# Kernel tuning notes

Hardware: AMD Instinct MI355X
Metric: run time of the kernel (lower is better)

The kernel has to match this reference:

```python
import jax, jax.numpy as jnp
import numpy as np

B, T, C = 2, 2048, 768
H, N_LEFT = 12, 6
D = C // H


def setup_inputs() -> dict:
    key = jax.random.key(0)
    ks = jax.random.split(key, 4)
    x = jax.random.normal(ks[0], (B, T, C), dtype=jnp.float32)
    attention_mask = jnp.ones((B, T), dtype=jnp.int32)
    Wqkv_w = jax.random.normal(ks[1], (3 * C, C), dtype=jnp.float32) * (C ** -0.5)
    Wqkv_b = jnp.zeros((3 * C,), dtype=jnp.float32)
    Wo_w = jax.random.normal(ks[2], (C, C), dtype=jnp.float32) * (C ** -0.5)
    Wo_b = jnp.zeros((C,), dtype=jnp.float32)
    return {"x": x, "attention_mask": attention_mask, "Wqkv_w": Wqkv_w,
            "Wqkv_b": Wqkv_b, "Wo_w": Wo_w, "Wo_b": Wo_b}


def _attend(q, k, v, mask):
    # q,k,v: [B,h,T,D]; mask: [B,1,T,T] additive
    s = jnp.einsum('bhqd,bhkd->bhqk', q, k) * (D ** -0.5) + mask
    a = jax.nn.softmax(s.astype(jnp.float32), axis=-1).astype(q.dtype)
    return jnp.einsum('bhqk,bhkd->bhqd', a, v)


def reference(x, attention_mask, Wqkv_w, Wqkv_b, Wo_w, Wo_b):
    neg = jnp.finfo(x.dtype).min
    # padding mask [B,1,1,T]: 0 where valid, neg where padded
    pad = (1.0 - attention_mask.astype(x.dtype))[:, None, None, :] * neg
    i = jnp.arange(T)
    tri = (i[None, :] > i[:, None]).astype(x.dtype) * neg   # triu(neg, 1)
    left_mask = tri[None, None] + pad                        # causal (look left)
    right_mask = tri.T[None, None] + pad                     # anti-causal (look right)

    qkv = (x @ Wqkv_w.T + Wqkv_b).reshape(B, T, 3, H, D)
    qkv = jnp.transpose(qkv, (0, 3, 2, 1, 4))                # [B,H,3,T,D]
    q, k, v = qkv[:, :, 0], qkv[:, :, 1], qkv[:, :, 2]

    lc = _attend(q[:, :N_LEFT], k[:, :N_LEFT], v[:, :N_LEFT], left_mask)
    rc = _attend(q[:, N_LEFT:], k[:, N_LEFT:], v[:, N_LEFT:], right_mask)
    ctx = jnp.concatenate([lc, rc], axis=1)                  # [B,H,T,D]
    ctx = jnp.transpose(ctx, (0, 2, 1, 3)).reshape(B, T, C)
    out = ctx @ Wo_w.T + Wo_b
    return out
```

## Files before the change

kernel.cpp:

```cpp
#include <hip/hip_runtime.h>


typedef unsigned short u16;
typedef __bf16 bf16x8 __attribute__((ext_vector_type(8)));
typedef float fx4 __attribute__((ext_vector_type(4)));
typedef unsigned short u16x8 __attribute__((ext_vector_type(8)));
typedef unsigned short u16x4 __attribute__((ext_vector_type(4)));
typedef _Float16 hx4 __attribute__((ext_vector_type(4)));
typedef __fp16 fp16x2 __attribute__((ext_vector_type(2)));

#define T_SEQ 2048
#define C_DIM 768
#define NHEAD 12
#define HDIM  64
#define NITEMS 768
#define LOG2E_8 0.18033688f

__device__ __forceinline__ u16 f2bf(float f) {
  unsigned u = __float_as_uint(f);
  u += 0x7fffu + ((u >> 16) & 1u);
  return (u16)(u >> 16);
}
__device__ __forceinline__ u16 f2h(float f) {
  union { _Float16 h; u16 u; } cv; cv.h = (_Float16)f; return cv.u;
}

__device__ __forceinline__ void gl2lds16(const u16* g, u16* l) {
  __builtin_amdgcn_global_load_lds(
      (const __attribute__((address_space(1))) void*)g,
      (__attribute__((address_space(3))) void*)l, 16, 0, 0);
}

__global__ void cvt_all_k(const float* __restrict__ x,
                          const float* __restrict__ wqkv,
                          const float* __restrict__ wo,
                          const int* __restrict__ am,
                          u16* __restrict__ out, float* __restrict__ mf,
                          unsigned* __restrict__ fbits, int* __restrict__ cnt) {
  if (blockIdx.x >= 2688) {
    int bid = blockIdx.x - 2688;
    int i = bid * blockDim.x + threadIdx.x;
    if (i < 4096) mf[i] = am[i] ? 0.f : -1e30f;
    if (bid == 16) {
      int t = threadIdx.x;
      if (t == 0) cnt[0] = 0;
      if (t < 64) {
        int bb = t >> 5, kt = t & 31;
        const int* seg = am + (bb << 11) + (kt << 6);
        int anyz = 0;
        for (int j = 0; j < 64; ++j) anyz |= (seg[j] == 0);
        unsigned long long bal = __ballot(anyz != 0);
        if (t == 0)  fbits[0] = (unsigned)(bal & 0xffffffffull);
        if (t == 32) fbits[1] = (unsigned)(bal >> 32);
      }
    }
    return;
  }
  int i = blockIdx.x * blockDim.x + threadIdx.x;
  int m = i / 96;
  int c8 = (i - m * 96) << 3;
  const float* src;
  if (m < 4096)       src = x    + (size_t)m * C_DIM + c8;
  else if (m < 6400)  src = wqkv + (size_t)(m - 4096) * C_DIM + c8;
  else                src = wo   + (size_t)(m - 6400) * C_DIM + c8;
  fx4 a = *(const fx4*)src, b = *(const fx4*)(src + 4);
  u16x8 o;
  #pragma unroll
  for (int j = 0; j < 4; ++j) { o[j] = f2bf(a[j]); o[4 + j] = f2bf(b[j]); }
  *(u16x8*)&out[(size_t)m * C_DIM + (c8 ^ ((m & 7) << 3))] = o;
}

__device__ __forceinline__ void gemm_core_128x128(const u16* __restrict__ A,
                                                  const u16* __restrict__ B,
                                                  int m0, int n0,
                                                  u16* As, u16* Bs,
                                                  fx4 acc[4][4]) {
  const int tid = threadIdx.x;
  const int lane = tid & 63, wv = tid >> 6;
  const int wm = (wv & 1) << 6, wn = (wv >> 1) << 6;
  const int lr = lane & 15, lg = lane >> 4;
  const int swk = (lr & 7) << 3;
  const int scol = (tid & 7) << 3;
  #pragma unroll
  for (int mt = 0; mt < 4; ++mt)
    #pragma unroll
    for (int nt = 0; nt < 4; ++nt) acc[mt][nt] = fx4{0.f, 0.f, 0.f, 0.f};

  #pragma unroll
  for (int p = 0; p < 4; ++p) {
    int row = (tid >> 3) + (p << 5);
    gl2lds16(&A[(size_t)(m0 + row) * C_DIM + scol], &As[(row << 6) + scol]);
    gl2lds16(&B[(size_t)(n0 + row) * C_DIM + scol], &Bs[(row << 6) + scol]);
  }

  int buf = 0;
  for (int k0 = 0; k0 < C_DIM; k0 += 64, buf ^= 1) {
    __syncthreads();
    if (k0 + 64 < C_DIM) {
      u16* Ad = &As[(buf ^ 1) << 13];
      u16* Bd = &Bs[(buf ^ 1) << 13];
      #pragma unroll
      for (int p = 0; p < 4; ++p) {
        int row = (tid >> 3) + (p << 5);
        gl2lds16(&A[(size_t)(m0 + row) * C_DIM + k0 + 64 + scol], &Ad[(row << 6) + scol]);
        gl2lds16(&B[(size_t)(n0 + row) * C_DIM + k0 + 64 + scol], &Bd[(row << 6) + scol]);
      }
    }
    const u16* Ab = &As[buf << 13];
    const u16* Bb = &Bs[buf << 13];
    #pragma unroll
    for (int kk = 0; kk < 64; kk += 32) {
      bf16x8 af[4], bfr[4];
      #pragma unroll
      for (int mt = 0; mt < 4; ++mt)
        af[mt] = *(const bf16x8*)&Ab[((wm + mt * 16 + lr) << 6) + ((kk + lg * 8) ^ swk)];
      #pragma unroll
      for (int nt = 0; nt < 4; ++nt)
        bfr[nt] = *(const bf16x8*)&Bb[((wn + nt * 16 + lr) << 6) + ((kk + lg * 8) ^ swk)];
      #pragma unroll
      for (int mt = 0; mt < 4; ++mt)
        #pragma unroll
        for (int nt = 0; nt < 4; ++nt)
          acc[mt][nt] = __builtin_amdgcn_mfma_f32_16x16x32_bf16(
              af[mt], bfr[nt], acc[mt][nt], 0, 0, 0);
    }
  }
}

__global__ __launch_bounds__(256) void gemm_qkv_k(
    const u16* __restrict__ A, const u16* __restrict__ B,
    const float* __restrict__ bias,
    u16* __restrict__ qb, u16* __restrict__ kswz, u16* __restrict__ vswz) {
  __shared__ __align__(16) u16 As[2][128 * 64];
  __shared__ __align__(16) u16 Bs[2][128 * 64];
  int m0 = blockIdx.y << 7, n0 = blockIdx.x << 7;
  fx4 acc[4][4];
  gemm_core_128x128(A, B, m0, n0, &As[0][0], &Bs[0][0], acc);

  const int tid = threadIdx.x, lane = tid & 63, wv = tid >> 6;
  const int wn = (wv >> 1) << 6;
  const int lr = lane & 15, lg = lane >> 4;
  const int part = n0 / 768;
  const int n0r = n0 - part * 768;
  u16* Sc = &Bs[0][0];

  #pragma unroll
  for (int mh = 0; mh < 2; ++mh) {
    __syncthreads();
    if ((wv & 1) == mh) {
      if (part < 2) {
        #pragma unroll
        for (int nt = 0; nt < 4; ++nt) {
          int nl = wn + nt * 16 + lr;
          float bv = bias[n0 + nl];
          #pragma unroll
          for (int mt = 0; mt < 4; ++mt) {
            #pragma unroll
            for (int r = 0; r < 4; ++r) {
              int m = mt * 16 + lg * 4 + r;
              Sc[(m << 7) + (nl ^ ((m & 15) << 2))] = f2bf(acc[mt][nt][r] + bv);
            }
          }
        }
      } else {
        #pragma unroll
        for (int nt = 0; nt < 4; ++nt) {
          int nl = wn + nt * 16 + lr;
          float bv = bias[n0 + nl];
          #pragma unroll
          for (int mt = 0; mt < 4; ++mt) {
            u16x4 pk;
            #pragma unroll
            for (int r = 0; r < 4; ++r) pk[r] = f2h(acc[mt][nt][r] + bv);
            int m4 = (mt << 2) + lg;
            *(u16x4*)&Sc[(nl << 6) + ((m4 ^ (nl & 15)) << 2)] = pk;
          }
        }
      }
    }
    __syncthreads();
    int meff = m0 + (mh << 6);
    int bb = meff >> 11, kt = (meff >> 6) & 31;
    if (part < 2) {
      int c4 = (tid & 31) << 2;
      int ng = n0r + c4;
      int hh = ng >> 6, d = ng & 63;
      int bh = bb * NHEAD + hh;
      #pragma unroll
      for (int p = 0; p < 8; ++p) {
        int m = (tid >> 5) + (p << 3);
        u16x4 v = *(const u16x4*)&Sc[(m << 7) + (c4 ^ ((m & 15) << 2))];
        if (part == 0) {
          int t = (meff & 2047) + m;
          *(u16x4*)&qb[(((size_t)bh << 11) + t) * HDIM + d] = v;
        } else {
          *(u16x4*)&kswz[((size_t)(bh * 32 + kt) << 12) + (m << 6) +
                         (d ^ ((m & 7) << 3))] = v;
        }
      }
    } else {
      int tr4 = tid & 15;
      #pragma unroll
      for (int p = 0; p < 8; ++p) {
        int nl = (tid >> 4) + (p << 4);
        int ng = n0r + nl;
        int hh = ng >> 6, d = ng & 63;
        u16x4 v = *(const u16x4*)&Sc[(nl << 6) + ((tr4 ^ (nl & 15)) << 2)];
        size_t tile = (size_t)((bb * NHEAD + hh) * 32 + kt) << 12;
        *(u16x4*)&vswz[tile + (d << 6) + ((tr4 ^ (d & 15)) << 2)] = v;
      }
    }
  }
}

__global__ __launch_bounds__(256) void gemm_out_k(
    const u16* __restrict__ A, const u16* __restrict__ B,
    const float* __restrict__ bias, float* __restrict__ out) {
  __shared__ __align__(16) u16 As[2][128 * 64];
  __shared__ __align__(16) u16 Bs[2][128 * 64];
  int m0 = blockIdx.y << 7, n0 = blockIdx.x << 7;
  fx4 acc[4][4];
  gemm_core_128x128(A, B, m0, n0, &As[0][0], &Bs[0][0], acc);

  const int tid = threadIdx.x, lane = tid & 63, wv = tid >> 6;
  const int wm = (wv & 1) << 6, wn = (wv >> 1) << 6;
  const int lr = lane & 15, lg = lane >> 4;
  #pragma unroll
  for (int nt = 0; nt < 4; ++nt) {
    int n = n0 + wn + nt * 16 + lr;
    float bv = bias[n];
    #pragma unroll
    for (int mt = 0; mt < 4; ++mt) {
      #pragma unroll
      for (int r = 0; r < 4; ++r) {
        int m = m0 + wm + mt * 16 + lg * 4 + r;
        out[(size_t)m * C_DIM + n] = acc[mt][nt][r] + bv;
      }
    }
  }
}

__global__ __launch_bounds__(256) void attn_k(
    const u16* __restrict__ q, const u16* __restrict__ kswz,
    const u16* __restrict__ vswz, const float* __restrict__ maskf,
    const unsigned* __restrict__ fbits,
    u16* __restrict__ ctx, int* __restrict__ counter) {
  __shared__ __align__(16) u16 Ks[2][4096];
  __shared__ __align__(16) u16 Vt[2][4096];
  __shared__ float Ls[4][64];
  __shared__ int s_w;

  const int tid = threadIdx.x, lane = tid & 63, wv = tid >> 6;
  const int lr = lane & 15, lg = lane >> 4;
  const int swk = (lr & 7) << 3;
  const int swv = (lr & 15) << 2;
  const int ke0 = ((wv * 16 + lr) << 6) + ((lg * 8) ^ swk);
  const int ke1 = ((wv * 16 + lr) << 6) + (((32 + lg * 8)) ^ swk);
  int vek[4];
  #pragma unroll
  for (int dt = 0; dt < 4; ++dt)
    vek[dt] = ((dt * 16 + lr) << 6) + ((wv * 16 + lg * 4) ^ swv);

  for (;;) {
    if (tid == 0) s_w = atomicAdd(counter, 1);
    __syncthreads();
    int w = s_w;
    if (w >= NITEMS) break;
    int qslot = w / 24, bh = w - qslot * 24;
    int bb = bh / NHEAD, h = bh - bb * NHEAD;
    bool causal = (h < 6);
    int qt = causal ? (31 - qslot) : qslot;
    int kt0 = causal ? 0 : qt;
    int kt1 = causal ? qt : 31;
    size_t tile_base = (size_t)(bh * 32) << 12;
    unsigned fb = fbits[bb];

    {
      const u16* kg = kswz + tile_base + ((size_t)kt0 << 12);
      const u16* vg = vswz + tile_base + ((size_t)kt0 << 12);
      #pragma unroll
      for (int c2 = 0; c2 < 2; ++c2) {
        int e = (wv << 10) + (c2 << 9) + (lane << 3);
        gl2lds16(kg + e, &Ks[0][e]);
        gl2lds16(vg + e, &Vt[0][e]);
      }
    }

    int q0 = qt << 6;
    size_t head_off = ((size_t)bh << 11) * HDIM;
    bf16x8 qf[4][2];
    #pragma unroll
    for (int g = 0; g < 4; ++g) {
      int qr = q0 + g * 16 + lr;
      qf[g][0] = *(const bf16x8*)&q[head_off + (size_t)qr * HDIM + lg * 8];
      qf[g][1] = *(const bf16x8*)&q[head_off + (size_t)qr * HDIM + 32 + lg * 8];
    }
    const float* mrow = maskf + (bb << 11);

    fx4 o[4][4];
    #pragma unroll
    for (int dt = 0; dt < 4; ++dt)
      #pragma unroll
      for (int g = 0; g < 4; ++g) o[dt][g] = fx4{0.f, 0.f, 0.f, 0.f};
    float l[4] = {0.f, 0.f, 0.f, 0.f};

    int buf = 0;
    for (int kt = kt0; kt <= kt1; ++kt, buf ^= 1) {
      __syncthreads();
      if (kt < kt1) {
        const u16* kg = kswz + tile_base + ((size_t)(kt + 1) << 12);
        const u16* vg = vswz + tile_base + ((size_t)(kt + 1) << 12);
        #pragma unroll
        for (int c2 = 0; c2 < 2; ++c2) {
          int e = (wv << 10) + (c2 << 9) + (lane << 3);
          gl2lds16(kg + e, &Ks[buf ^ 1][e]);
          gl2lds16(vg + e, &Vt[buf ^ 1][e]);
        }
      }

      const u16* kb = &Ks[buf][0];
      const u16* vbl = &Vt[buf][0];

      bf16x8 kf0 = *(const bf16x8*)&kb[ke0];
      bf16x8 kf1 = *(const bf16x8*)&kb[ke1];
      fx4 st[4];
      #pragma unroll
      for (int g = 0; g < 4; ++g) {
        fx4 z = fx4{0.f, 0.f, 0.f, 0.f};
        z = __builtin_amdgcn_mfma_f32_16x16x32_bf16(kf0, qf[g][0], z, 0, 0, 0);
        st[g] = __builtin_amdgcn_mfma_f32_16x16x32_bf16(kf1, qf[g][1], z, 0, 0, 0);
      }

      int kb0 = (kt << 6) + wv * 16 + lg * 4;
      if (kt == qt) {
        fx4 mv = *(const fx4*)&mrow[kb0];
        #pragma unroll
        for (int g = 0; g < 4; ++g) {
          int qr = q0 + g * 16 + lr;
          #pragma unroll
          for (int r = 0; r < 4; ++r) {
            float arg = st[g][r] * LOG2E_8 + mv[r];
            int kabs = kb0 + r;
            bool dead = causal ? (kabs > qr) : (kabs < qr);
            arg = dead ? -1e30f : arg;
            float p = __builtin_amdgcn_exp2f(arg);
            st[g][r] = p;
            l[g] += p;
          }
        }
      } else if ((fb >> kt) & 1u) {
        fx4 mv = *(const fx4*)&mrow[kb0];
        #pragma unroll
        for (int g = 0; g < 4; ++g)
          #pragma unroll
          for (int r = 0; r < 4; ++r) {
            float p = __builtin_amdgcn_exp2f(st[g][r] * LOG2E_8 + mv[r]);
            st[g][r] = p;
            l[g] += p;
          }
      } else {
        #pragma unroll
        for (int g = 0; g < 4; ++g)
          #pragma unroll
          for (int r = 0; r < 4; ++r) {
            float p = __builtin_amdgcn_exp2f(st[g][r] * LOG2E_8);
            st[g][r] = p;
            l[g] += p;
          }
      }

      hx4 pf[4];
      #pragma unroll
      for (int g = 0; g < 4; ++g) {
        union { hx4 v; fp16x2 hh[2]; } pu;
        pu.hh[0] = __builtin_amdgcn_cvt_pkrtz(st[g][0], st[g][1]);
        pu.hh[1] = __builtin_amdgcn_cvt_pkrtz(st[g][2], st[g][3]);
        pf[g] = pu.v;
      }
      #pragma unroll
      for (int dt = 0; dt < 4; ++dt) {
        hx4 vf = *(const hx4*)&vbl[vek[dt]];
        #pragma unroll
        for (int g = 0; g < 4; ++g)
          o[dt][g] = __builtin_amdgcn_mfma_f32_16x16x16f16(vf, pf[g], o[dt][g], 0, 0, 0);
      }
    }

    __syncthreads();
    #pragma unroll
    for (int g = 0; g < 4; ++g) {
      l[g] += __shfl_xor(l[g], 16, 64);
      l[g] += __shfl_xor(l[g], 32, 64);
    }
    if (lg == 0) {
      #pragma unroll
      for (int g = 0; g < 4; ++g) Ls[wv][g * 16 + lr] = l[g];
    }
    float* r0 = (float*)&Ks[0][0];
    float* r1 = (float*)&Vt[0][0];
    float* rg = (wv & 1) ? r1 : r0;
    if (wv < 2) {
      #pragma unroll
      for (int dt = 0; dt < 4; ++dt)
        #pragma unroll
        for (int g = 0; g < 4; ++g) {
          int qq = g * 16 + lr, c = dt * 4 + lg;
          *(fx4*)&rg[(qq << 6) + ((c ^ (qq & 15)) << 2)] = o[dt][g];
        }
    }
    __syncthreads();
    if (wv >= 2) {
      #pragma unroll
      for (int dt = 0; dt < 4; ++dt)
        #pragma unroll
        for (int g = 0; g < 4; ++g) {
          int qq = g * 16 + lr, c = dt * 4 + lg;
          float* p = &rg[(qq << 6) + ((c ^ (qq & 15)) << 2)];
          fx4 cur = *(const fx4*)p;
          cur += o[dt][g];
          *(fx4*)p = cur;
        }
    }
    __syncthreads();
    {
      int qq = (wv << 4) + lr;
      float linv = 1.f / (Ls[0][qq] + Ls[1][qq] + Ls[2][qq] + Ls[3][qq]);
      int tq = q0 + qq;
      size_t rowb = ((size_t)(bb << 11) + tq) * C_DIM;
      int csw = (tq & 7) << 3;
      #pragma unroll
      for (int j = 0; j < 4; ++j) {
        int c = (lg << 2) + j;
        int off = (qq << 6) + ((c ^ (qq & 15)) << 2);
        fx4 v0 = *(const fx4*)&r0[off];
        fx4 v1 = *(const fx4*)&r1[off];
        u16x4 pk;
        #pragma unroll
        for (int r = 0; r < 4; ++r) pk[r] = f2bf((v0[r] + v1[r]) * linv);
        int colb = h * HDIM + (c << 2);
        *(u16x4*)&ctx[rowb + (colb ^ csw)] = pk;
      }
    }
  }
}

extern "C" void kernel_launch(void* const* d_in, const int* in_sizes, int n_in,
                              void* d_out, int out_size, void* d_ws, size_t ws_size,
                              hipStream_t stream) {
  const float* x     = (const float*)d_in[0];
  const int*   amask = (const int*)d_in[1];
  const float* wqkv  = (const float*)d_in[2];
  const float* bqkv  = (const float*)d_in[3];
  const float* wo    = (const float*)d_in[4];
  const float* bo    = (const float*)d_in[5];
  float* out = (float*)d_out;

  char* ws = (char*)d_ws;
  u16*      xb    = (u16*)(ws + 0);
  u16*      wqkvb = (u16*)(ws + 6291456);
  u16*      wob   = (u16*)(ws + 9830400);
  u16*      qb    = (u16*)(ws + 11010048);
  u16*      kswz  = (u16*)(ws + 17301504);
  u16*      vswz  = (u16*)(ws + 23592960);
  u16*      ctxb  = (u16*)(ws + 29884416);
  float*    maskf = (float*)(ws + 36175872);
  int*      cnt   = (int*)(ws + 36192256);
  unsigned* fbits = (unsigned*)(ws + 36192320);

  cvt_all_k<<<2705, 256, 0, stream>>>(x, wqkv, wo, amask, xb,
                                      maskf, fbits, cnt);

  gemm_qkv_k<<<dim3(18, 32), 256, 0, stream>>>(xb, wqkvb, bqkv, qb, kswz, vswz);
  attn_k<<<512, 256, 0, stream>>>(qb, kswz, vswz, maskf, fbits, ctxb, cnt);
  gemm_out_k<<<dim3(6, 32), 256, 0, stream>>>(ctxb, wob, bo, out);
}
```

Measured before the change: 165.9 us.

## Replace LDS-staged GEMMs with direct global-to-register MFMA loads and smaller output tiles

Both projection GEMMs stop staging A/B tiles through double-buffered LDS and instead load MFMA fragments straight from global memory into registers, relying on L1/L2 for reuse. Since LDS staging is gone, the XOR swizzle on the bf16 converted inputs and on the ctx output is removed. The output GEMM moves to 64x64 tiles with four times as many blocks to fill more CUs. The QKV epilogue now writes both half-tiles to separate LDS buffers at once, which cuts a sync round. The cost is uncoalesced, strided global fragment loads and more redundant global traffic, with no explicit prefetch overlap.

```diff
diff --git a/kernel.cpp b/kernel.cpp
--- a/kernel.cpp
+++ b/kernel.cpp
@@ -67,118 +67,88 @@
   u16x8 o;
   #pragma unroll
   for (int j = 0; j < 4; ++j) { o[j] = f2bf(a[j]); o[4 + j] = f2bf(b[j]); }
-  *(u16x8*)&out[(size_t)m * C_DIM + (c8 ^ ((m & 7) << 3))] = o;
-}
-
-__device__ __forceinline__ void gemm_core_128x128(const u16* __restrict__ A,
-                                                  const u16* __restrict__ B,
-                                                  int m0, int n0,
-                                                  u16* As, u16* Bs,
-                                                  fx4 acc[4][4]) {
-  const int tid = threadIdx.x;
-  const int lane = tid & 63, wv = tid >> 6;
-  const int wm = (wv & 1) << 6, wn = (wv >> 1) << 6;
-  const int lr = lane & 15, lg = lane >> 4;
-  const int swk = (lr & 7) << 3;
-  const int scol = (tid & 7) << 3;
-  #pragma unroll
-  for (int mt = 0; mt < 4; ++mt)
-    #pragma unroll
-    for (int nt = 0; nt < 4; ++nt) acc[mt][nt] = fx4{0.f, 0.f, 0.f, 0.f};
-
-  #pragma unroll
-  for (int p = 0; p < 4; ++p) {
-    int row = (tid >> 3) + (p << 5);
-    gl2lds16(&A[(size_t)(m0 + row) * C_DIM + scol], &As[(row << 6) + scol]);
-    gl2lds16(&B[(size_t)(n0 + row) * C_DIM + scol], &Bs[(row << 6) + scol]);
-  }
-
-  int buf = 0;
-  for (int k0 = 0; k0 < C_DIM; k0 += 64, buf ^= 1) {
-    __syncthreads();
-    if (k0 + 64 < C_DIM) {
-      u16* Ad = &As[(buf ^ 1) << 13];
-      u16* Bd = &Bs[(buf ^ 1) << 13];
-      #pragma unroll
-      for (int p = 0; p < 4; ++p) {
-        int row = (tid >> 3) + (p << 5);
-        gl2lds16(&A[(size_t)(m0 + row) * C_DIM + k0 + 64 + scol], &Ad[(row << 6) + scol]);
-        gl2lds16(&B[(size_t)(n0 + row) * C_DIM + k0 + 64 + scol], &Bd[(row << 6) + scol]);
-      }
-    }
-    const u16* Ab = &As[buf << 13];
-    const u16* Bb = &Bs[buf << 13];
-    #pragma unroll
-    for (int kk = 0; kk < 64; kk += 32) {
-      bf16x8 af[4], bfr[4];
-      #pragma unroll
-      for (int mt = 0; mt < 4; ++mt)
-        af[mt] = *(const bf16x8*)&Ab[((wm + mt * 16 + lr) << 6) + ((kk + lg * 8) ^ swk)];
-      #pragma unroll
-      for (int nt = 0; nt < 4; ++nt)
-        bfr[nt] = *(const bf16x8*)&Bb[((wn + nt * 16 + lr) << 6) + ((kk + lg * 8) ^ swk)];
-      #pragma unroll
-      for (int mt = 0; mt < 4; ++mt)
-        #pragma unroll
-        for (int nt = 0; nt < 4; ++nt)
-          acc[mt][nt] = __builtin_amdgcn_mfma_f32_16x16x32_bf16(
-              af[mt], bfr[nt], acc[mt][nt], 0, 0, 0);
-    }
-  }
+  *(u16x8*)&out[(size_t)m * C_DIM + c8] = o;
 }
 
 __global__ __launch_bounds__(256) void gemm_qkv_k(
     const u16* __restrict__ A, const u16* __restrict__ B,
     const float* __restrict__ bias,
     u16* __restrict__ qb, u16* __restrict__ kswz, u16* __restrict__ vswz) {
-  __shared__ __align__(16) u16 As[2][128 * 64];
-  __shared__ __align__(16) u16 Bs[2][128 * 64];
+  __shared__ __align__(16) u16 Sc2[2][128 * 64];
   int m0 = blockIdx.y << 7, n0 = blockIdx.x << 7;
+  const int tid = threadIdx.x, lane = tid & 63, wv = tid >> 6;
+  const int wm = (wv & 1) << 6, wn = (wv >> 1) << 6;
+  const int lr = lane & 15, lg = lane >> 4;
+
+  const u16* arow[4];
+  const u16* brow[4];
+  #pragma unroll
+  for (int t = 0; t < 4; ++t) {
+    arow[t] = A + (size_t)(m0 + wm + t * 16 + lr) * C_DIM + lg * 8;
+    brow[t] = B + (size_t)(n0 + wn + t * 16 + lr) * C_DIM + lg * 8;
+  }
+
   fx4 acc[4][4];
-  gemm_core_128x128(A, B, m0, n0, &As[0][0], &Bs[0][0], acc);
-
-  const int tid = threadIdx.x, lane = tid & 63, wv = tid >> 6;
-  const int wn = (wv >> 1) << 6;
-  const int lr = lane & 15, lg = lane >> 4;
+  #pragma unroll
+  for (int mt = 0; mt < 4; ++mt)
+    #pragma unroll
+    for (int nt = 0; nt < 4; ++nt) acc[mt][nt] = fx4{0.f, 0.f, 0.f, 0.f};
+
+  #pragma unroll 4
+  for (int k = 0; k < C_DIM; k += 32) {
+    bf16x8 af[4], bfr[4];
+    #pragma unroll
+    for (int mt = 0; mt < 4; ++mt) af[mt] = *(const bf16x8*)(arow[mt] + k);
+    #pragma unroll
+    for (int nt = 0; nt < 4; ++nt) bfr[nt] = *(const bf16x8*)(brow[nt] + k);
+    #pragma unroll
+    for (int mt = 0; mt < 4; ++mt)
+      #pragma unroll
+      for (int nt = 0; nt < 4; ++nt)
+        acc[mt][nt] = __builtin_amdgcn_mfma_f32_16x16x32_bf16(
+            af[mt], bfr[nt], acc[mt][nt], 0, 0, 0);
+  }
+
   const int part = n0 / 768;
   const int n0r = n0 - part * 768;
-  u16* Sc = &Bs[0][0];
+  const int myh = wv & 1;
+  const int wnl = (wv >> 1) << 6;
+  u16* Smy = &Sc2[myh][0];
+
+  if (part < 2) {
+    #pragma unroll
+    for (int nt = 0; nt < 4; ++nt) {
+      int nl = wnl + nt * 16 + lr;
+      float bv = bias[n0 + nl];
+      #pragma unroll
+      for (int mt = 0; mt < 4; ++mt) {
+        #pragma unroll
+        for (int r = 0; r < 4; ++r) {
+          int m = mt * 16 + lg * 4 + r;
+          Smy[(m << 7) + (nl ^ ((m & 15) << 2))] = f2bf(acc[mt][nt][r] + bv);
+        }
+      }
+    }
+  } else {
+    #pragma unroll
+    for (int nt = 0; nt < 4; ++nt) {
+      int nl = wnl + nt * 16 + lr;
+      float bv = bias[n0 + nl];
+      #pragma unroll
+      for (int mt = 0; mt < 4; ++mt) {
+        u16x4 pk;
+        #pragma unroll
+        for (int r = 0; r < 4; ++r) pk[r] = f2h(acc[mt][nt][r] + bv);
+        int m4 = (mt << 2) + lg;
+        *(u16x4*)&Smy[(nl << 6) + ((m4 ^ (nl & 15)) << 2)] = pk;
+      }
+    }
+  }
+  __syncthreads();
 
   #pragma unroll
   for (int mh = 0; mh < 2; ++mh) {
-    __syncthreads();
-    if ((wv & 1) == mh) {
-      if (part < 2) {
-        #pragma unroll
-        for (int nt = 0; nt < 4; ++nt) {
-          int nl = wn + nt * 16 + lr;
-          float bv = bias[n0 + nl];
-          #pragma unroll
-          for (int mt = 0; mt < 4; ++mt) {
-            #pragma unroll
-            for (int r = 0; r < 4; ++r) {
-              int m = mt * 16 + lg * 4 + r;
-              Sc[(m << 7) + (nl ^ ((m & 15) << 2))] = f2bf(acc[mt][nt][r] + bv);
-            }
-          }
-        }
-      } else {
-        #pragma unroll
-        for (int nt = 0; nt < 4; ++nt) {
-          int nl = wn + nt * 16 + lr;
-          float bv = bias[n0 + nl];
-          #pragma unroll
-          for (int mt = 0; mt < 4; ++mt) {
-            u16x4 pk;
-            #pragma unroll
-            for (int r = 0; r < 4; ++r) pk[r] = f2h(acc[mt][nt][r] + bv);
-            int m4 = (mt << 2) + lg;
-            *(u16x4*)&Sc[(nl << 6) + ((m4 ^ (nl & 15)) << 2)] = pk;
-          }
-        }
-      }
-    }
-    __syncthreads();
+    const u16* Sc = &Sc2[mh][0];
     int meff = m0 + (mh << 6);
     int bb = meff >> 11, kt = (meff >> 6) & 31;
     if (part < 2) {
@@ -216,21 +186,46 @@
 __global__ __launch_bounds__(256) void gemm_out_k(
     const u16* __restrict__ A, const u16* __restrict__ B,
     const float* __restrict__ bias, float* __restrict__ out) {
-  __shared__ __align__(16) u16 As[2][128 * 64];
-  __shared__ __align__(16) u16 Bs[2][128 * 64];
-  int m0 = blockIdx.y << 7, n0 = blockIdx.x << 7;
-  fx4 acc[4][4];
-  gemm_core_128x128(A, B, m0, n0, &As[0][0], &Bs[0][0], acc);
-
+  int m0 = blockIdx.y << 6, n0 = blockIdx.x << 6;
   const int tid = threadIdx.x, lane = tid & 63, wv = tid >> 6;
-  const int wm = (wv & 1) << 6, wn = (wv >> 1) << 6;
+  const int wm = (wv & 1) << 5, wn = (wv >> 1) << 5;
   const int lr = lane & 15, lg = lane >> 4;
-  #pragma unroll
-  for (int nt = 0; nt < 4; ++nt) {
+
+  const u16* arow[2];
+  const u16* brow[2];
+  #pragma unroll
+  for (int t = 0; t < 2; ++t) {
+    arow[t] = A + (size_t)(m0 + wm + t * 16 + lr) * C_DIM + lg * 8;
+    brow[t] = B + (size_t)(n0 + wn + t * 16 + lr) * C_DIM + lg * 8;
+  }
+
+  fx4 acc[2][2];
+  #pragma unroll
+  for (int mt = 0; mt < 2; ++mt)
+    #pragma unroll
+    for (int nt = 0; nt < 2; ++nt) acc[mt][nt] = fx4{0.f, 0.f, 0.f, 0.f};
+
+  #pragma unroll 6
+  for (int k = 0; k < C_DIM; k += 32) {
+    bf16x8 af[2], bfr[2];
+    #pragma unroll
+    for (int mt = 0; mt < 2; ++mt) af[mt] = *(const bf16x8*)(arow[mt] + k);
+    #pragma unroll
+    for (int nt = 0; nt < 2; ++nt) bfr[nt] = *(const bf16x8*)(brow[nt] + k);
+    #pragma unroll
+    for (int mt = 0; mt < 2; ++mt)
+      #pragma unroll
+      for (int nt = 0; nt < 2; ++nt)
+        acc[mt][nt] = __builtin_amdgcn_mfma_f32_16x16x32_bf16(
+            af[mt], bfr[nt], acc[mt][nt], 0, 0, 0);
+  }
+
+  #pragma unroll
+  for (int nt = 0; nt < 2; ++nt) {
     int n = n0 + wn + nt * 16 + lr;
     float bv = bias[n];
     #pragma unroll
-    for (int mt = 0; mt < 4; ++mt) {
+    for (int mt = 0; mt < 2; ++mt) {
       #pragma unroll
       for (int r = 0; r < 4; ++r) {
         int m = m0 + wm + mt * 16 + lg * 4 + r;
@@ -427,7 +422,6 @@
       float linv = 1.f / (Ls[0][qq] + Ls[1][qq] + Ls[2][qq] + Ls[3][qq]);
       int tq = q0 + qq;
       size_t rowb = ((size_t)(bb << 11) + tq) * C_DIM;
-      int csw = (tq & 7) << 3;
       #pragma unroll
       for (int j = 0; j < 4; ++j) {
         int c = (lg << 2) + j;
@@ -438,7 +432,7 @@
         #pragma unroll
         for (int r = 0; r < 4; ++r) pk[r] = f2bf((v0[r] + v1[r]) * linv);
         int colb = h * HDIM + (c << 2);
-        *(u16x4*)&ctx[rowb + (colb ^ csw)] = pk;
+        *(u16x4*)&ctx[rowb + colb] = pk;
       }
     }
   }
@@ -472,5 +466,5 @@
 
   gemm_qkv_k<<<dim3(18, 32), 256, 0, stream>>>(xb, wqkvb, bqkv, qb, kswz, vswz);
   attn_k<<<512, 256, 0, stream>>>(qb, kswz, vswz, maskf, fbits, ctxb, cnt);
-  gemm_out_k<<<dim3(6, 32), 256, 0, stream>>>(ctxb, wob, bo, out);
-}
+  gemm_out_k<<<dim3(12, 64), 256, 0, stream>>>(ctxb, wob, bo, out);
+}
```

After: 225.1 us. +35.7%, slower.
